# Kernel optimization log

Measured on AMD Instinct MI355X. Metric: run time of the kernel, lower is better.

The kernel has to match this reference:

```python
import jax, jax.numpy as jnp
import numpy as np

NOT_EPSILON = 1.0
B, S, D = 1, 512, 256


def swishmax(x, axis):
    xexp = x * jnp.exp(x - jnp.max(x, axis=axis, keepdims=True))
    return xexp / (jnp.sum(jnp.abs(xexp), axis=axis, keepdims=True) + NOT_EPSILON)


def setup_inputs() -> dict:
    key = jax.random.key(0)
    ks = jax.random.split(key, 13)
    scale = 1.0 / np.sqrt(D)
    mk = lambda k: jax.random.uniform(k, (D, D), jnp.float32, -scale, scale)
    mb = lambda k: jax.random.uniform(k, (D,), jnp.float32, -scale, scale)
    return {
        "query_tokens": jax.random.normal(ks[0], (B, S, D), jnp.float32),
        "key_tokens": jax.random.normal(ks[1], (B, S, D), jnp.float32),
        "value_tokens": jax.random.normal(ks[2], (B, S, D), jnp.float32),
        "Wk": mk(ks[3]), "bk": mb(ks[4]),
        "Wq": mk(ks[5]), "bq": mb(ks[6]),
        "Wva": mk(ks[7]), "bva": mb(ks[8]),
        "Wl": mk(ks[9]), "bl": mb(ks[10]),
        "Wvo": mk(ks[11]), "bvo": mb(ks[12]),
    }


def reference(query_tokens, key_tokens, value_tokens,
              Wk, bk, Wq, bq, Wva, bva, Wl, bl, Wvo, bvo):
    # residual linear transforms of tokens
    k = key_tokens + key_tokens @ Wk + bk        # [B,S,D]
    q = query_tokens + query_tokens @ Wq + bq    # [B,S,D]
    # batchify: key -> [B,Sk,1,D], query -> [B,1,Sq,D]; outer-product scores
    attention_raw = k[:, :, None, :] * q[:, None, :, :]          # [B,Sk,Sq,D]
    attention_logits = attention_raw + attention_raw @ Wl + bl   # DxD linear on raw scores
    attention_scale = swishmax(attention_logits, axis=-2)        # normalize over query axis (dim -shape_dims)
    v = value_tokens + value_tokens @ Wva + bva  # [B,S,D]
    values_scaled = v[:, :, None, :] * attention_scale           # [B,Sk,Sq,D]
    value_sum = values_scaled.sum(axis=-3)                       # reduce key axis -> [B,Sq,D]
    value_out = value_sum + value_sum @ Wvo + bvo
    return value_out
```

## Files before the change

kernel.cpp:

```cpp
#include <hip/hip_runtime.h>
#include <math.h>

#define S_LEN 512
#define D_DIM 256
#define SLICE (S_LEN * D_DIM)

typedef _Float16 half8  __attribute__((ext_vector_type(8)));
typedef _Float16 half4v __attribute__((ext_vector_type(4)));
typedef float   floatx4 __attribute__((ext_vector_type(4)));

__global__ __launch_bounds__(256) void prep_wl(const float* __restrict__ Wl,
                                               _Float16* __restrict__ WlhT)
{
    const int d = blockIdx.x, e = threadIdx.x;
    float v = Wl[e * D_DIM + d] + (e == d ? 1.0f : 0.0f);
    WlhT[d * D_DIM + e] = (_Float16)v;
}

__global__ __launch_bounds__(256) void linres3(
    const float* __restrict__ xk, const float* __restrict__ Wk,
    const float* __restrict__ bk, _Float16* __restrict__ yk16,
    const float* __restrict__ xq, const float* __restrict__ Wq,
    const float* __restrict__ bq, _Float16* __restrict__ yq16,
    const float* __restrict__ xv, const float* __restrict__ Wv,
    const float* __restrict__ bv, float* __restrict__ yv)
{
    __shared__ float xs[4][D_DIM];
    const int r0 = blockIdx.x * 4;
    const int sel = blockIdx.y;
    const float* x = sel == 0 ? xk : (sel == 1 ? xq : xv);
    const float* W = sel == 0 ? Wk : (sel == 1 ? Wq : Wv);
    const float* b = sel == 0 ? bk : (sel == 1 ? bq : bv);

    const int tid = threadIdx.x;
    #pragma unroll
    for (int t = 0; t < 4; ++t) xs[t][tid] = x[(r0 + t) * D_DIM + tid];
    __syncthreads();
    const float bv_ = b[tid];
    float acc[4];
    #pragma unroll
    for (int i = 0; i < 4; ++i) acc[i] = xs[i][tid] + bv_;
    #pragma unroll 4
    for (int e = 0; e < D_DIM; ++e) {
        const float w = W[e * D_DIM + tid];
        #pragma unroll
        for (int i = 0; i < 4; ++i) acc[i] += xs[i][e] * w;
    }
    if (sel == 2) {
        #pragma unroll
        for (int i = 0; i < 4; ++i) yv[(r0 + i) * D_DIM + tid] = acc[i];
    } else {
        _Float16* y16 = sel == 0 ? yk16 : yq16;
        #pragma unroll
        for (int i = 0; i < 4; ++i) y16[(r0 + i) * D_DIM + tid] = (_Float16)acc[i];
    }
}

__global__ __launch_bounds__(256) void linres_sum(
    const float* __restrict__ po, const float* __restrict__ W,
    const float* __restrict__ b, float* __restrict__ y)
{
    __shared__ float xs[4][D_DIM];
    const int tid = threadIdx.x;
    const int r0  = blockIdx.x * 4;
    #pragma unroll
    for (int t = 0; t < 4; ++t) {
        float s = 0.f;
        #pragma unroll
        for (int c = 0; c < 16; ++c)
            s += po[(size_t)c * SLICE + (r0 + t) * D_DIM + tid];
        xs[t][tid] = s;
    }
    __syncthreads();
    const float bv_ = b[tid];
    float acc[4];
    #pragma unroll
    for (int i = 0; i < 4; ++i) acc[i] = xs[i][tid] + bv_;
    #pragma unroll 4
    for (int e = 0; e < D_DIM; ++e) {
        const float w = W[e * D_DIM + tid];
        #pragma unroll
        for (int i = 0; i < 4; ++i) acc[i] += xs[i][e] * w;
    }
    #pragma unroll
    for (int i = 0; i < 4; ++i) y[(r0 + i) * D_DIM + tid] = acc[i];
}

__device__ __forceinline__ void stage_q(const _Float16* __restrict__ qh,
                                        _Float16* __restrict__ Afrag,
                                        int sq0, int tid)
{
    const int i   = tid & 63;
    const int qtr = tid >> 6;
    const int mt = i >> 4, l16 = i & 15;
    const half8* src = (const half8*)(qh + (size_t)(sq0 + i) * D_DIM + qtr * 64);
    #pragma unroll
    for (int u = 0; u < 8; ++u) {
        const int eb   = qtr * 8 + u;
        const int kk   = eb >> 2, quad = eb & 3;
        const int addr16 = (mt * 8 + kk) * 64 + quad * 16 + l16;
        *(half8*)(Afrag + addr16 * 8) = src[u];
    }
}

__device__ __forceinline__ void stage_q32(const _Float16* __restrict__ qh,
                                          _Float16* __restrict__ Afrag,
                                          int sq0, int tid)
{
    const int i   = tid & 31;
    const int oct = tid >> 5;
    const int mt = i >> 4, l16 = i & 15;
    const half8* src = (const half8*)(qh + (size_t)(sq0 + i) * D_DIM);
    #pragma unroll
    for (int u = 0; u < 4; ++u) {
        const int eb   = oct * 4 + u;
        const int kk   = eb >> 2, quad = eb & 3;
        const int addr16 = (mt * 8 + kk) * 64 + quad * 16 + l16;
        *(half8*)(Afrag + addr16 * 8) = src[eb];
    }
}

__global__ __launch_bounds__(256, 2) void stats_mfma(
    const _Float16* __restrict__ qh, const _Float16* __restrict__ kh,
    const _Float16* __restrict__ WlhT, const float* __restrict__ bl,
    float* __restrict__ pm, float* __restrict__ ps)
{
    __shared__ _Float16 Afrag[32 * 64 * 8];

    const int tid  = threadIdx.x;
    const int lane = tid & 63, wave = tid >> 6;
    const int quad = lane >> 4, l16 = lane & 15;
    const int sqt  = blockIdx.x, sq0 = sqt * 64;
    const int dw   = blockIdx.y * 128 + wave * 32;
    const int sk0  = blockIdx.z * 16;

    stage_q(qh, Afrag, sq0, tid);

    half8 wl[2][8];
    #pragma unroll
    for (int nt = 0; nt < 2; ++nt) {
        const int d = dw + nt * 16 + l16;
        #pragma unroll
        for (int kk = 0; kk < 8; ++kk)
            wl[nt][kk] = *(const half8*)(WlhT + (size_t)d * D_DIM + kk * 32 + quad * 8);
    }
    float bl_r[2];
    #pragma unroll
    for (int nt = 0; nt < 2; ++nt)
        bl_r[nt] = bl[dw + nt * 16 + l16];

    __syncthreads();

    #pragma unroll 1
    for (int s = 0; s < 16; ++s) {
        const int sk = sk0 + s;
        floatx4 acc[4][2];
        #pragma unroll
        for (int mt = 0; mt < 4; ++mt)
            #pragma unroll
            for (int nt = 0; nt < 2; ++nt)
                acc[mt][nt] = (floatx4){0.f, 0.f, 0.f, 0.f};

        #pragma unroll
        for (int kk = 0; kk < 8; ++kk) {
            const half8 k8 = *(const half8*)(kh + (size_t)sk * D_DIM + kk * 32 + quad * 8);
            half8 af[4], bf[2];
            #pragma unroll
            for (int mt = 0; mt < 4; ++mt)
                af[mt] = *(const half8*)(Afrag + ((mt * 8 + kk) * 64 + lane) * 8);
            #pragma unroll
            for (int nt = 0; nt < 2; ++nt)
                bf[nt] = wl[nt][kk] * k8;
            #pragma unroll
            for (int mt = 0; mt < 4; ++mt)
                #pragma unroll
                for (int nt = 0; nt < 2; ++nt)
                    acc[mt][nt] = __builtin_amdgcn_mfma_f32_16x16x32_f16(
                        af[mt], bf[nt], acc[mt][nt], 0, 0, 0);
        }

        #pragma unroll
        for (int nt = 0; nt < 2; ++nt) {
            float Lv[4][4];
            float tmax = -1e30f;
            #pragma unroll
            for (int mt = 0; mt < 4; ++mt)
                #pragma unroll
                for (int r = 0; r < 4; ++r) {
                    const float L = acc[mt][nt][r] + bl_r[nt];
                    Lv[mt][r] = L;
                    tmax = fmaxf(tmax, L);
                }
            float tsum = 0.f;
            #pragma unroll
            for (int mt = 0; mt < 4; ++mt)
                #pragma unroll
                for (int r = 0; r < 4; ++r)
                    tsum += fabsf(Lv[mt][r]) * __expf(Lv[mt][r] - tmax);

            float m = tmax, ss = tsum;
            #pragma unroll
            for (int mask = 16; mask <= 32; mask <<= 1) {
                float m2 = __shfl_xor(m, mask, 64);
                float s2 = __shfl_xor(ss, mask, 64);
                float M  = fmaxf(m, m2);
                ss = ss * __expf(m - M) + s2 * __expf(m2 - M);
                m = M;
            }
            if (quad == 0) {
                const int d = dw + nt * 16 + l16;
                pm[((size_t)sqt * S_LEN + sk) * D_DIM + d] = m;
                ps[((size_t)sqt * S_LEN + sk) * D_DIM + d] = ss;
            }
        }
    }
}

__global__ __launch_bounds__(256) void reduce_ms(
    const float* __restrict__ pm, const float* __restrict__ ps,
    float* __restrict__ mbuf, float* __restrict__ sbuf)
{
    const int idx = blockIdx.x * 256 + threadIdx.x;
    float mv[8], sv[8];
    #pragma unroll
    for (int t = 0; t < 8; ++t) {
        mv[t] = pm[(size_t)t * SLICE + idx];
        sv[t] = ps[(size_t)t * SLICE + idx];
    }
    float M = mv[0];
    #pragma unroll
    for (int t = 1; t < 8; ++t) M = fmaxf(M, mv[t]);
    float ss = 0.f;
    #pragma unroll
    for (int t = 0; t < 8; ++t) ss += sv[t] * __expf(mv[t] - M);
    mbuf[idx] = M;
    sbuf[idx] = ss;
}

__global__ __launch_bounds__(256, 2) void accum_mfma(
    const _Float16* __restrict__ qh, const _Float16* __restrict__ kh,
    const _Float16* __restrict__ WlhT, const float* __restrict__ bl,
    const float* __restrict__ mbuf, const float* __restrict__ sbuf,
    const float* __restrict__ vbuf, float* __restrict__ po)
{
    __shared__ _Float16 Afrag[16 * 64 * 8];

    const int tid  = threadIdx.x;
    const int lane = tid & 63, wave = tid >> 6;
    const int quad = lane >> 4, l16 = lane & 15;
    const int sq0  = blockIdx.x * 32;
    const int dw   = blockIdx.y * 128 + wave * 32;
    const int chunk = blockIdx.z;
    const int sk0  = chunk * 32;

    stage_q32(qh, Afrag, sq0, tid);

    half8 wl[2][8];
    #pragma unroll
    for (int nt = 0; nt < 2; ++nt) {
        const int d = dw + nt * 16 + l16;
        #pragma unroll
        for (int kk = 0; kk < 8; ++kk)
            wl[nt][kk] = *(const half8*)(WlhT + (size_t)d * D_DIM + kk * 32 + quad * 8);
    }
    float bl_r[2];
    #pragma unroll
    for (int nt = 0; nt < 2; ++nt)
        bl_r[nt] = bl[dw + nt * 16 + l16];

    floatx4 o[2][2];
    #pragma unroll
    for (int mt = 0; mt < 2; ++mt)
        #pragma unroll
        for (int nt = 0; nt < 2; ++nt)
            o[mt][nt] = (floatx4){0.f, 0.f, 0.f, 0.f};

    __syncthreads();

    #pragma unroll 1
    for (int s = 0; s < 32; ++s) {
        const int sk = sk0 + s;

        float m_r2[2], w_r2[2];
        #pragma unroll
        for (int nt = 0; nt < 2; ++nt) {
            const int d = dw + nt * 16 + l16;
            m_r2[nt] = mbuf[(size_t)sk * D_DIM + d];
            const float sden = sbuf[(size_t)sk * D_DIM + d];
            const float vv   = vbuf[(size_t)sk * D_DIM + d];
            w_r2[nt] = vv / (sden + 1.0f);
        }

        floatx4 acc[2][2];
        #pragma unroll
        for (int mt = 0; mt < 2; ++mt)
            #pragma unroll
            for (int nt = 0; nt < 2; ++nt)
                acc[mt][nt] = (floatx4){0.f, 0.f, 0.f, 0.f};

        #pragma unroll
        for (int kk = 0; kk < 8; ++kk) {
            const half8 k8 = *(const half8*)(kh + (size_t)sk * D_DIM + kk * 32 + quad * 8);
            half8 af[2], bf[2];
            #pragma unroll
            for (int mt = 0; mt < 2; ++mt)
                af[mt] = *(const half8*)(Afrag + ((mt * 8 + kk) * 64 + lane) * 8);
            #pragma unroll
            for (int nt = 0; nt < 2; ++nt)
                bf[nt] = wl[nt][kk] * k8;
            #pragma unroll
            for (int mt = 0; mt < 2; ++mt)
                #pragma unroll
                for (int nt = 0; nt < 2; ++nt)
                    acc[mt][nt] = __builtin_amdgcn_mfma_f32_16x16x32_f16(
                        af[mt], bf[nt], acc[mt][nt], 0, 0, 0);
        }

        #pragma unroll
        for (int nt = 0; nt < 2; ++nt) {
            const float m_r = m_r2[nt];
            const float w_r = w_r2[nt];
            #pragma unroll
            for (int mt = 0; mt < 2; ++mt)
                #pragma unroll
                for (int r = 0; r < 4; ++r) {
                    const float L = acc[mt][nt][r] + bl_r[nt];
                    const float t = __expf(L - m_r);
                    o[mt][nt][r] += w_r * (L * t);
                }
        }
    }

    float* dst = po + (size_t)chunk * SLICE;
    #pragma unroll
    for (int mt = 0; mt < 2; ++mt)
        #pragma unroll
        for (int nt = 0; nt < 2; ++nt)
            #pragma unroll
            for (int r = 0; r < 4; ++r) {
                const int row = sq0 + mt * 16 + quad * 4 + r;
                const int col = dw + nt * 16 + l16;
                dst[(size_t)row * D_DIM + col] = o[mt][nt][r];
            }
}

extern "C" void kernel_launch(void* const* d_in, const int* in_sizes, int n_in,
                              void* d_out, int out_size, void* d_ws, size_t ws_size,
                              hipStream_t stream)
{
    const float* query = (const float*)d_in[0];
    const float* key   = (const float*)d_in[1];
    const float* value = (const float*)d_in[2];
    const float* Wk  = (const float*)d_in[3];
    const float* bk  = (const float*)d_in[4];
    const float* Wq  = (const float*)d_in[5];
    const float* bq  = (const float*)d_in[6];
    const float* Wva = (const float*)d_in[7];
    const float* bva = (const float*)d_in[8];
    const float* Wl  = (const float*)d_in[9];
    const float* bl  = (const float*)d_in[10];
    const float* Wvo = (const float*)d_in[11];
    const float* bvo = (const float*)d_in[12];

    const int MAT = SLICE;
    float* ws   = (float*)d_ws;
    float* vbuf = ws + 2 * MAT;
    float* mbuf = ws + 3 * MAT;
    float* sbuf = ws + 4 * MAT;
    _Float16* WlhT = (_Float16*)(ws + 6 * MAT);
    _Float16* kh   = (_Float16*)(ws + 6 * MAT + 32768);
    _Float16* qh   = kh + MAT;
    float* pm  = ws + 6 * MAT + 32768 + 2 * 65536;
    float* ps  = pm + 8 * MAT;
    float* po  = pm;
    float* out = (float*)d_out;

    prep_wl<<<256, 256, 0, stream>>>(Wl, WlhT);
    linres3<<<dim3(128, 3), 256, 0, stream>>>(key, Wk, bk, kh,
                                              query, Wq, bq, qh,
                                              value, Wva, bva, vbuf);

    stats_mfma<<<dim3(8, 2, 32), 256, 0, stream>>>(qh, kh, WlhT, bl, pm, ps);
    reduce_ms<<<512, 256, 0, stream>>>(pm, ps, mbuf, sbuf);
    accum_mfma<<<dim3(16, 2, 16), 256, 0, stream>>>(qh, kh, WlhT, bl,
                                                    mbuf, sbuf, vbuf, po);

    linres_sum<<<128, 256, 0, stream>>>(po, Wvo, bvo, out);
}
```

Baseline: 215.2 us.

## Hoist query A-fragments into registers and narrow stats tile per wave

Both MFMA kernels now load the staged query fragments from LDS into registers once, before the sk loop, instead of reloading them on every inner k step. The stats kernel is also narrowed to one 16-column d tile per wave, and its grid doubles in y to keep full coverage. Its key row is prefetched into registers at the start of each iteration. This removes repeated LDS traffic and adds parallelism, at the cost of higher VGPR pressure (32 half8 registers in stats), which may reduce occupancy under the launch bounds.

```diff
diff --git a/kernel.cpp b/kernel.cpp
--- a/kernel.cpp
+++ b/kernel.cpp
@@ -131,87 +131,78 @@
     const int lane = tid & 63, wave = tid >> 6;
     const int quad = lane >> 4, l16 = lane & 15;
     const int sqt  = blockIdx.x, sq0 = sqt * 64;
-    const int dw   = blockIdx.y * 128 + wave * 32;
+    const int dw   = blockIdx.y * 64 + wave * 16;
     const int sk0  = blockIdx.z * 16;
 
     stage_q(qh, Afrag, sq0, tid);
 
-    half8 wl[2][8];
-    #pragma unroll
-    for (int nt = 0; nt < 2; ++nt) {
-        const int d = dw + nt * 16 + l16;
+    half8 wl[8];
+    const int d = dw + l16;
+    #pragma unroll
+    for (int kk = 0; kk < 8; ++kk)
+        wl[kk] = *(const half8*)(WlhT + (size_t)d * D_DIM + kk * 32 + quad * 8);
+    const float bl_r = bl[d];
+
+    __syncthreads();
+
+    half8 afr[4][8];
+    #pragma unroll
+    for (int mt = 0; mt < 4; ++mt)
         #pragma unroll
         for (int kk = 0; kk < 8; ++kk)
-            wl[nt][kk] = *(const half8*)(WlhT + (size_t)d * D_DIM + kk * 32 + quad * 8);
-    }
-    float bl_r[2];
-    #pragma unroll
-    for (int nt = 0; nt < 2; ++nt)
-        bl_r[nt] = bl[dw + nt * 16 + l16];
-
-    __syncthreads();
+            afr[mt][kk] = *(const half8*)(Afrag + ((mt * 8 + kk) * 64 + lane) * 8);
 
     #pragma unroll 1
     for (int s = 0; s < 16; ++s) {
         const int sk = sk0 + s;
-        floatx4 acc[4][2];
+
+        half8 k8a[8];
+        #pragma unroll
+        for (int kk = 0; kk < 8; ++kk)
+            k8a[kk] = *(const half8*)(kh + (size_t)sk * D_DIM + kk * 32 + quad * 8);
+
+        floatx4 acc[4];
         #pragma unroll
         for (int mt = 0; mt < 4; ++mt)
-            #pragma unroll
-            for (int nt = 0; nt < 2; ++nt)
-                acc[mt][nt] = (floatx4){0.f, 0.f, 0.f, 0.f};
+            acc[mt] = (floatx4){0.f, 0.f, 0.f, 0.f};
 
         #pragma unroll
         for (int kk = 0; kk < 8; ++kk) {
-            const half8 k8 = *(const half8*)(kh + (size_t)sk * D_DIM + kk * 32 + quad * 8);
-            half8 af[4], bf[2];
+            const half8 bf = wl[kk] * k8a[kk];
             #pragma unroll
             for (int mt = 0; mt < 4; ++mt)
-                af[mt] = *(const half8*)(Afrag + ((mt * 8 + kk) * 64 + lane) * 8);
-            #pragma unroll
-            for (int nt = 0; nt < 2; ++nt)
-                bf[nt] = wl[nt][kk] * k8;
-            #pragma unroll
-            for (int mt = 0; mt < 4; ++mt)
-                #pragma unroll
-                for (int nt = 0; nt < 2; ++nt)
-                    acc[mt][nt] = __builtin_amdgcn_mfma_f32_16x16x32_f16(
-                        af[mt], bf[nt], acc[mt][nt], 0, 0, 0);
-        }
-
-        #pragma unroll
-        for (int nt = 0; nt < 2; ++nt) {
-            float Lv[4][4];
-            float tmax = -1e30f;
-            #pragma unroll
-            for (int mt = 0; mt < 4; ++mt)
-                #pragma unroll
-                for (int r = 0; r < 4; ++r) {
-                    const float L = acc[mt][nt][r] + bl_r[nt];
-                    Lv[mt][r] = L;
-                    tmax = fmaxf(tmax, L);
-                }
-            float tsum = 0.f;
-            #pragma unroll
-            for (int mt = 0; mt < 4; ++mt)
-                #pragma unroll
-                for (int r = 0; r < 4; ++r)
-                    tsum += fabsf(Lv[mt][r]) * __expf(Lv[mt][r] - tmax);
-
-            float m = tmax, ss = tsum;
-            #pragma unroll
-            for (int mask = 16; mask <= 32; mask <<= 1) {
-                float m2 = __shfl_xor(m, mask, 64);
-                float s2 = __shfl_xor(ss, mask, 64);
-                float M  = fmaxf(m, m2);
-                ss = ss * __expf(m - M) + s2 * __expf(m2 - M);
-                m = M;
+                acc[mt] = __builtin_amdgcn_mfma_f32_16x16x32_f16(
+                    afr[mt][kk], bf, acc[mt], 0, 0, 0);
+        }
+
+        float tmax = -1e30f;
+        #pragma unroll
+        for (int mt = 0; mt < 4; ++mt)
+            #pragma unroll
+            for (int r = 0; r < 4; ++r) {
+                const float L = acc[mt][r] + bl_r;
+                acc[mt][r] = L;
+                tmax = fmaxf(tmax, L);
             }
-            if (quad == 0) {
-                const int d = dw + nt * 16 + l16;
-                pm[((size_t)sqt * S_LEN + sk) * D_DIM + d] = m;
-                ps[((size_t)sqt * S_LEN + sk) * D_DIM + d] = ss;
-            }
+        float tsum = 0.f;
+        #pragma unroll
+        for (int mt = 0; mt < 4; ++mt)
+            #pragma unroll
+            for (int r = 0; r < 4; ++r)
+                tsum += fabsf(acc[mt][r]) * __expf(acc[mt][r] - tmax);
+
+        float m = tmax, ss = tsum;
+        #pragma unroll
+        for (int mask = 16; mask <= 32; mask <<= 1) {
+            float m2 = __shfl_xor(m, mask, 64);
+            float s2 = __shfl_xor(ss, mask, 64);
+            float M  = fmaxf(m, m2);
+            ss = ss * __expf(m - M) + s2 * __expf(m2 - M);
+            m = M;
+        }
+        if (quad == 0) {
+            pm[((size_t)sqt * S_LEN + sk) * D_DIM + d] = m;
+            ps[((size_t)sqt * S_LEN + sk) * D_DIM + d] = ss;
         }
     }
 }
@@ -268,14 +259,21 @@
     for (int nt = 0; nt < 2; ++nt)
         bl_r[nt] = bl[dw + nt * 16 + l16];
 
+    __syncthreads();
+
+    half8 afr[2][8];
+    #pragma unroll
+    for (int mt = 0; mt < 2; ++mt)
+        #pragma unroll
+        for (int kk = 0; kk < 8; ++kk)
+            afr[mt][kk] = *(const half8*)(Afrag + ((mt * 8 + kk) * 64 + lane) * 8);
+
     floatx4 o[2][2];
     #pragma unroll
     for (int mt = 0; mt < 2; ++mt)
         #pragma unroll
         for (int nt = 0; nt < 2; ++nt)
             o[mt][nt] = (floatx4){0.f, 0.f, 0.f, 0.f};
-
-    __syncthreads();
 
     #pragma unroll 1
     for (int s = 0; s < 32; ++s) {
@@ -301,10 +299,7 @@
         #pragma unroll
         for (int kk = 0; kk < 8; ++kk) {
             const half8 k8 = *(const half8*)(kh + (size_t)sk * D_DIM + kk * 32 + quad * 8);
-            half8 af[2], bf[2];
-            #pragma unroll
-            for (int mt = 0; mt < 2; ++mt)
-                af[mt] = *(const half8*)(Afrag + ((mt * 8 + kk) * 64 + lane) * 8);
+            half8 bf[2];
             #pragma unroll
             for (int nt = 0; nt < 2; ++nt)
                 bf[nt] = wl[nt][kk] * k8;
@@ -313,7 +308,7 @@
                 #pragma unroll
                 for (int nt = 0; nt < 2; ++nt)
                     acc[mt][nt] = __builtin_amdgcn_mfma_f32_16x16x32_f16(
-                        af[mt], bf[nt], acc[mt][nt], 0, 0, 0);
+                        afr[mt][kk], bf[nt], acc[mt][nt], 0, 0, 0);
         }
 
         #pragma unroll
@@ -380,7 +375,7 @@
                                               query, Wq, bq, qh,
                                               value, Wva, bva, vbuf);
 
-    stats_mfma<<<dim3(8, 2, 32), 256, 0, stream>>>(qh, kh, WlhT, bl, pm, ps);
+    stats_mfma<<<dim3(8, 4, 32), 256, 0, stream>>>(qh, kh, WlhT, bl, pm, ps);
     reduce_ms<<<512, 256, 0, stream>>>(pm, ps, mbuf, sbuf);
     accum_mfma<<<dim3(16, 2, 16), 256, 0, stream>>>(qh, kh, WlhT, bl,
                                                     mbuf, sbuf, vbuf, po);
```

Result: slower. 222.0 us (+3.2%).
